# Kernel optimization log

Hardware: AMD Instinct MI355X
Metric: run time of the kernel (lower is better)

## Reference

```python
import jax, jax.numpy as jnp
import numpy as np

DIM = 1024
NUM_HEADS = 16
HEAD_DIM = DIM // NUM_HEADS


def setup_inputs() -> dict:
    key = jax.random.key(0)
    ks = jax.random.split(key, 6)
    B, N, C = 2, 2048, DIM
    s = 1.0 / np.sqrt(C)
    return {
        "x": jax.random.normal(ks[0], (B, N, C), dtype=jnp.float32),
        "Wq": jax.random.normal(ks[1], (C, C), dtype=jnp.float32) * s,
        "Wk": jax.random.normal(ks[2], (C, C), dtype=jnp.float32) * s,
        "Wv": jax.random.normal(ks[3], (C, C), dtype=jnp.float32) * s,
        "Wproj": jax.random.normal(ks[4], (C, C), dtype=jnp.float32) * s,
        "bproj": jax.random.normal(ks[5], (C,), dtype=jnp.float32) * 0.01,
    }


def reference(x, Wq, Wk, Wv, Wproj, bproj):
    B, N, C = x.shape
    H, D = NUM_HEADS, HEAD_DIM
    scale = D ** -0.5
    # Linear (torch convention: y = x @ W.T), then split heads -> [B, H, N, D]
    q = (x @ Wq.T).reshape(B, N, H, D).transpose(0, 2, 1, 3)
    k = (x @ Wk.T).reshape(B, N, H, D).transpose(0, 2, 1, 3)
    v = (x @ Wv.T).reshape(B, N, H, D).transpose(0, 2, 1, 3)
    attn = jnp.einsum("bhnd,bhmd->bhnm", q, k) * scale  # [B,H,N,N]
    attn = jax.nn.softmax(attn, axis=-1)
    out = jnp.einsum("bhnm,bhmd->bhnd", attn, v)  # [B,H,N,D]
    out = out.transpose(0, 2, 1, 3).reshape(B, N, C)
    return out @ Wproj.T + bproj
```

## Files before the change

kernel.cpp:

```cpp
#include <hip/hip_runtime.h>
#include <stdint.h>

typedef unsigned short u16;
typedef unsigned int u32;

typedef __bf16 bf16x8 __attribute__((ext_vector_type(8)));
typedef float f32x4 __attribute__((ext_vector_type(4)));

#define LOG2E_SCALE 0.18033688011112042f

static __device__ __forceinline__ u16 f2bf(float f) {
  union { float f; u32 u; } v; v.f = f;
  u32 r = v.u + 0x7fffu + ((v.u >> 16) & 1u);
  return (u16)(r >> 16);
}
static __device__ __forceinline__ u32 pk2(float a, float b) {
  u32 r;
  asm("v_cvt_pk_bf16_f32 %0, %1, %2" : "=v"(r) : "v"(a), "v"(b));
  return r;
}
static __device__ __forceinline__ float fexp2(float x) {
  return __builtin_amdgcn_exp2f(x);
}
static __device__ __forceinline__ float blo(u32 u) {
  union { u32 u; float f; } v; v.u = u << 16; return v.f;
}
static __device__ __forceinline__ float bhi(u32 u) {
  union { u32 u; float f; } v; v.u = u & 0xffff0000u; return v.f;
}

static __device__ __forceinline__ void gl_lds16(const void* g, void* l) {
  __builtin_amdgcn_global_load_lds(
      (const __attribute__((address_space(1))) u32*)g,
      (__attribute__((address_space(3))) u32*)l, 16, 0, 0);
}

__global__ void cast_kernel(const float* __restrict__ x, const float* __restrict__ wq,
                            const float* __restrict__ wk, const float* __restrict__ wv,
                            const float* __restrict__ wp,
                            u16* __restrict__ xb, u16* __restrict__ wqb, u16* __restrict__ wkb,
                            u16* __restrict__ wvb, u16* __restrict__ wpb) {
  const float* src; u16* dst; int n;
  switch (blockIdx.y) {
    case 0: src = x;  dst = xb;  n = 4194304; break;
    case 1: src = wq; dst = wqb; n = 1048576; break;
    case 2: src = wk; dst = wkb; n = 1048576; break;
    case 3: src = wv; dst = wvb; n = 1048576; break;
    default: src = wp; dst = wpb; n = 1048576; break;
  }
  int i = (blockIdx.x * 256 + threadIdx.x) * 8;
  if (i >= n) return;
  float4 a = *(const float4*)(src + i);
  float4 b = *(const float4*)(src + i + 4);
  uint4 o;
  o.x = pk2(a.x, a.y); o.y = pk2(a.z, a.w);
  o.z = pk2(b.x, b.y); o.w = pk2(b.z, b.w);
  *(uint4*)(dst + i) = o;
}

__global__ __launch_bounds__(256, 3) void gemm_qkv(
    const u16* __restrict__ A, const u16* __restrict__ Bq, const u16* __restrict__ Bk,
    const u16* __restrict__ Bv, u16* __restrict__ oQ, u16* __restrict__ oK,
    u16* __restrict__ oVt)
{
  constexpr int K = 1024;
  __shared__ u16 As[128 * 32];
  __shared__ u16 Bs[128 * 32];
  __shared__ float tbuf[4][16 * 68];

  const int tid  = threadIdx.x;
  const int lane = tid & 63;
  const int wave = tid >> 6;
  const int cl   = lane & 15;
  const int g    = lane >> 4;
  const int wm   = (wave >> 1) * 64;
  const int wn   = (wave & 1) * 64;
  const int bm   = blockIdx.y * 128;
  const int bn   = blockIdx.x * 128;
  const int z    = blockIdx.z;
  const u16* B = (z == 0 ? Bq : (z == 1 ? Bk : Bv));

  f32x4 zero4 = {0.f, 0.f, 0.f, 0.f};
  f32x4 acc[4][4];
#pragma unroll
  for (int i = 0; i < 4; i++)
#pragma unroll
    for (int j = 0; j < 4; j++) acc[i][j] = zero4;

  const int srow = tid >> 2;
  const int sch  = (tid & 3) ^ ((srow >> 1) & 3);
  const char* aG = (const char*)(A + (size_t)(bm + srow) * K) + sch * 16;
  const char* bG = (const char*)(B + (size_t)(bn + srow) * K) + sch * 16;
  char* aL = (char*)As + tid * 16;
  char* bL = (char*)Bs + tid * 16;
  const size_t rstep = (size_t)64 * K * 2;

  const int swz = (cl >> 1) & 3;

  for (int k0 = 0; k0 < K; k0 += 32) {
    gl_lds16(aG + k0 * 2, aL);
    gl_lds16(aG + rstep + k0 * 2, aL + 4096);
    gl_lds16(bG + k0 * 2, bL);
    gl_lds16(bG + rstep + k0 * 2, bL + 4096);
    __syncthreads();

    bf16x8 af[4], bf[4];
#pragma unroll
    for (int i = 0; i < 4; i++)
      af[i] = *(const bf16x8*)(As + (wm + i * 16 + cl) * 32 + ((g ^ swz) & 3) * 8);
#pragma unroll
    for (int j = 0; j < 4; j++)
      bf[j] = *(const bf16x8*)(Bs + (wn + j * 16 + cl) * 32 + ((g ^ swz) & 3) * 8);
#pragma unroll
    for (int i = 0; i < 4; i++)
#pragma unroll
      for (int j = 0; j < 4; j++)
        acc[i][j] = __builtin_amdgcn_mfma_f32_16x16x32_bf16(af[i], bf[j], acc[i][j], 0, 0, 0);
    __syncthreads();
  }

  const int rq = g * 4;
  if (z <= 1) {
    u16* o = z ? oK : oQ;
#pragma unroll
    for (int i = 0; i < 4; i++)
#pragma unroll
      for (int j = 0; j < 4; j++)
#pragma unroll
        for (int r = 0; r < 4; r++) {
          int gm = bm + wm + i * 16 + rq + r;
          int gn = bn + wn + j * 16 + cl;
          int b = gm >> 11, ns = gm & 2047;
          int h = gn >> 6,  d  = gn & 63;
          o[(((size_t)(b * 16 + h)) * 2048 + ns) * 64 + d] = f2bf(acc[i][j][r]);
        }
  } else {
    float* tb = tbuf[wave];
#pragma unroll
    for (int j = 0; j < 4; j++) {
      asm volatile("s_waitcnt lgkmcnt(0)" ::: "memory");
#pragma unroll
      for (int i = 0; i < 4; i++)
        *(f32x4*)(tb + cl * 68 + i * 16 + rq) = acc[i][j];
      asm volatile("s_waitcnt lgkmcnt(0)" ::: "memory");
#pragma unroll
      for (int half = 0; half < 2; half++) {
        int dd = lane >> 2, p = (lane & 3) + half * 4;
        f32x4 x0 = *(const f32x4*)(tb + dd * 68 + p * 8);
        f32x4 x1 = *(const f32x4*)(tb + dd * 68 + p * 8 + 4);
        uint4 pkd;
        pkd.x = pk2(x0[0], x0[1]); pkd.y = pk2(x0[2], x0[3]);
        pkd.z = pk2(x1[0], x1[1]); pkd.w = pk2(x1[2], x1[3]);
        int gn = bn + wn + j * 16 + dd;
        int gm = bm + wm + p * 8;
        int b = gm >> 11, nn = gm & 2047;
        int h = gn >> 6,  dl = gn & 63;
        *(uint4*)(oVt + (((size_t)(b * 16 + h)) * 64 + dl) * 2048 + nn) = pkd;
      }
    }
  }
}

__global__ __launch_bounds__(256, 4) void attn_kernel(
    const u16* __restrict__ Q, const u16* __restrict__ Km,
    const u16* __restrict__ Vt, u16* __restrict__ Op, float* __restrict__ lp)
{
  __shared__ u16 ks[2][64 * 64];
  __shared__ u16 vs[2][64 * 64];
  __shared__ u16 ps[128 * 32];

  const int tid  = threadIdx.x;
  const int lane = tid & 63;
  const int wave = tid >> 6;
  const int cl   = lane & 15;
  const int g    = lane >> 4;
  const int bh   = blockIdx.x;
  const int qt   = blockIdx.y;
  const int sp   = blockIdx.z;

  const char* kS = (const char*)Km + (size_t)bh * 2048 * 128 + (size_t)sp * 1024 * 128;
  const char* vS = (const char*)Vt + (size_t)bh * 64 * 4096 + (size_t)sp * 1024 * 2;

  const u16* qbase = Q + ((size_t)bh * 2048 + qt * 128 + wave * 32) * 64;
  bf16x8 qf[2][2];
#pragma unroll
  for (int i = 0; i < 2; i++)
#pragma unroll
    for (int h = 0; h < 2; h++)
      qf[i][h] = *(const bf16x8*)(qbase + (i * 16 + cl) * 64 + h * 32 + g * 8);

  auto stage_k = [&](int t) {
    const char* kT = kS + (size_t)t * 8192;
    char* dst = (char*)ks[t & 1];
#pragma unroll
    for (int r = 0; r < 2; r++) {
      int c = r * 256 + tid;
      int kv = c >> 3, s = c & 7;
      gl_lds16(kT + kv * 128 + (((s ^ kv) & 7) * 16), dst + c * 16);
    }
  };
  auto stage_v = [&](int t) {
    const char* vT = vS + (size_t)t * 128;
    char* dst = (char*)vs[t & 1];
#pragma unroll
    for (int r = 0; r < 2; r++) {
      int c = r * 256 + tid;
      int d = c >> 3, s = c & 7;
      gl_lds16(vT + (size_t)d * 4096 + (((s ^ d) & 7) * 16), dst + c * 16);
    }
  };

  stage_k(0);
  stage_v(0);

  f32x4 zero4 = {0.f, 0.f, 0.f, 0.f};
  f32x4 o_acc[2][4];
#pragma unroll
  for (int i = 0; i < 2; i++)
#pragma unroll
    for (int j = 0; j < 4; j++) o_acc[i][j] = zero4;
  float li[2] = {0.f, 0.f};

  for (int t = 0; t < 16; ++t) {
    __syncthreads();
    if (t < 15) { stage_k(t + 1); stage_v(t + 1); }

    const u16* kb = ks[t & 1];
    const u16* vb = vs[t & 1];

    f32x4 st[4][2];
#pragma unroll
    for (int j = 0; j < 4; j++) { st[j][0] = zero4; st[j][1] = zero4; }
#pragma unroll
    for (int h = 0; h < 2; h++) {
#pragma unroll
      for (int j = 0; j < 4; j++) {
        bf16x8 kf = *(const bf16x8*)(kb + (j * 16 + cl) * 64 + (((h * 4 + g) ^ (cl & 7)) & 7) * 8);
        st[j][0] = __builtin_amdgcn_mfma_f32_16x16x32_bf16(kf, qf[0][h], st[j][0], 0, 0, 0);
        st[j][1] = __builtin_amdgcn_mfma_f32_16x16x32_bf16(kf, qf[1][h], st[j][1], 0, 0, 0);
      }
    }

#pragma unroll
    for (int i = 0; i < 2; i++) {
      float rs = 0.f;
#pragma unroll
      for (int j = 0; j < 4; j++)
#pragma unroll
        for (int r = 0; r < 4; r++) {
          float p = fexp2(st[j][i][r] * LOG2E_SCALE);
          st[j][i][r] = p;
          rs += p;
        }
      rs += __shfl_xor(rs, 16, 64);
      rs += __shfl_xor(rs, 32, 64);
      li[i] += rs;
    }

#pragma unroll
    for (int h32 = 0; h32 < 2; h32++) {
#pragma unroll
      for (int i = 0; i < 2; i++) {
        int q = wave * 32 + i * 16 + cl;
#pragma unroll
        for (int jj = 0; jj < 2; jj++) {
          int j = h32 * 2 + jj;
          int ch = jj * 2 + (g >> 1);
          int slot = (ch ^ (cl & 3)) & 3;
          uint2 w;
          w.x = pk2(st[j][i][0], st[j][i][1]);
          w.y = pk2(st[j][i][2], st[j][i][3]);
          *(uint2*)((char*)ps + q * 64 + slot * 16 + (g & 1) * 8) = w;
        }
      }
      bf16x8 pf[2], vf[4];
#pragma unroll
      for (int i = 0; i < 2; i++)
        pf[i] = *(const bf16x8*)((const char*)ps + (wave * 32 + i * 16 + cl) * 64 +
                                 ((g ^ (cl & 3)) & 3) * 16);
#pragma unroll
      for (int j = 0; j < 4; j++)
        vf[j] = *(const bf16x8*)(vb + (j * 16 + cl) * 64 + (((h32 * 4 + g) ^ (cl & 7)) & 7) * 8);
#pragma unroll
      for (int i = 0; i < 2; i++)
#pragma unroll
        for (int j = 0; j < 4; j++)
          o_acc[i][j] = __builtin_amdgcn_mfma_f32_16x16x32_bf16(pf[i], vf[j], o_acc[i][j], 0, 0, 0);
    }
  }

  const int b = bh >> 4, hh = bh & 15;
  u16* Os = Op + (size_t)sp * 4194304;
  float* ls = lp + sp * 65536;
#pragma unroll
  for (int i = 0; i < 2; i++) {
    if (g == 0) ls[bh * 2048 + qt * 128 + wave * 32 + i * 16 + cl] = li[i];
#pragma unroll
    for (int r = 0; r < 4; r++) {
      int row = qt * 128 + wave * 32 + i * 16 + g * 4 + r;
      u16* orow = Os + ((size_t)b * 2048 + row) * 1024 + hh * 64;
#pragma unroll
      for (int j = 0; j < 4; j++)
        orow[j * 16 + cl] = f2bf(o_acc[i][j][r]);
    }
  }
}

__global__ void reduce_o(const u16* __restrict__ Op, const float* __restrict__ lp,
                         u16* __restrict__ Ow) {
  int t = blockIdx.x * 256 + threadIdx.x;
  int idx = t * 8;
  int b   = idx >> 21;
  int rem = idx & 2097151;
  int row = rem >> 10;
  int h   = (rem & 1023) >> 6;
  int lidx = (b * 16 + h) * 2048 + row;
  float inv = 1.0f / (lp[lidx] + lp[65536 + lidx]);
  uint4 a = *(const uint4*)(Op + idx);
  uint4 c = *(const uint4*)(Op + 4194304 + idx);
  uint4 o;
  o.x = pk2((blo(a.x) + blo(c.x)) * inv, (bhi(a.x) + bhi(c.x)) * inv);
  o.y = pk2((blo(a.y) + blo(c.y)) * inv, (bhi(a.y) + bhi(c.y)) * inv);
  o.z = pk2((blo(a.z) + blo(c.z)) * inv, (bhi(a.z) + bhi(c.z)) * inv);
  o.w = pk2((blo(a.w) + blo(c.w)) * inv, (bhi(a.w) + bhi(c.w)) * inv);
  *(uint4*)(Ow + idx) = o;
}

__global__ __launch_bounds__(256, 4) void proj_gemm(
    const u16* __restrict__ A, const u16* __restrict__ B,
    float* __restrict__ out, const float* __restrict__ bias)
{
  constexpr int K = 1024;
  __shared__ u16 As[64 * 32];
  __shared__ u16 Bs[128 * 32];

  const int tid  = threadIdx.x;
  const int lane = tid & 63;
  const int wave = tid >> 6;
  const int cl   = lane & 15;
  const int g    = lane >> 4;
  const int wm   = (wave >> 1) * 32;
  const int wn   = (wave & 1) * 64;
  const int bm   = blockIdx.y * 64;
  const int bn   = blockIdx.x * 128;

  f32x4 zero4 = {0.f, 0.f, 0.f, 0.f};
  f32x4 acc[2][4];
#pragma unroll
  for (int i = 0; i < 2; i++)
#pragma unroll
    for (int j = 0; j < 4; j++) acc[i][j] = zero4;

  const int srow = tid >> 2;
  const int sch  = (tid & 3) ^ ((srow >> 1) & 3);
  const char* aG = (const char*)(A + (size_t)(bm + srow) * K) + sch * 16;
  const char* bG = (const char*)(B + (size_t)(bn + srow) * K) + sch * 16;
  char* aL = (char*)As + tid * 16;
  char* bL = (char*)Bs + tid * 16;
  const size_t rstep = (size_t)64 * K * 2;

  const int swz = (cl >> 1) & 3;

  for (int k0 = 0; k0 < K; k0 += 32) {
    gl_lds16(aG + k0 * 2, aL);
    gl_lds16(bG + k0 * 2, bL);
    gl_lds16(bG + rstep + k0 * 2, bL + 4096);
    __syncthreads();

    bf16x8 af[2], bf[4];
#pragma unroll
    for (int i = 0; i < 2; i++)
      af[i] = *(const bf16x8*)(As + (wm + i * 16 + cl) * 32 + ((g ^ swz) & 3) * 8);
#pragma unroll
    for (int j = 0; j < 4; j++)
      bf[j] = *(const bf16x8*)(Bs + (wn + j * 16 + cl) * 32 + ((g ^ swz) & 3) * 8);
#pragma unroll
    for (int i = 0; i < 2; i++)
#pragma unroll
      for (int j = 0; j < 4; j++)
        acc[i][j] = __builtin_amdgcn_mfma_f32_16x16x32_bf16(af[i], bf[j], acc[i][j], 0, 0, 0);
    __syncthreads();
  }

  const int rq = g * 4;
#pragma unroll
  for (int i = 0; i < 2; i++)
#pragma unroll
    for (int j = 0; j < 4; j++)
#pragma unroll
      for (int r = 0; r < 4; r++) {
        int gm = bm + wm + i * 16 + rq + r;
        int gn = bn + wn + j * 16 + cl;
        out[(size_t)gm * 1024 + gn] = acc[i][j][r] + bias[gn];
      }
}

extern "C" void kernel_launch(void* const* d_in, const int* in_sizes, int n_in,
                              void* d_out, int out_size, void* d_ws, size_t ws_size,
                              hipStream_t stream) {
  const float* x     = (const float*)d_in[0];
  const float* Wq    = (const float*)d_in[1];
  const float* Wk    = (const float*)d_in[2];
  const float* Wv    = (const float*)d_in[3];
  const float* Wp    = (const float*)d_in[4];
  const float* bproj = (const float*)d_in[5];

  u16* ws  = (u16*)d_ws;
  u16* xb  = ws;
  u16* wqb = xb + 4194304;
  u16* wkb = wqb + 1048576;
  u16* wvb = wkb + 1048576;
  u16* wpb = wvb + 1048576;
  u16* Qw  = wpb + 1048576;
  u16* Kw  = Qw + 4194304;
  u16* Vw  = Kw + 4194304;
  u16* Ow  = Vw + 4194304;
  u16* Opart = Ow + 4194304;
  float* lpart = (float*)(Opart + 8388608);
  (void)in_sizes; (void)n_in; (void)out_size; (void)ws_size;

  cast_kernel<<<dim3(2048, 5), 256, 0, stream>>>(x, Wq, Wk, Wv, Wp, xb, wqb, wkb, wvb, wpb);
  gemm_qkv<<<dim3(8, 32, 3), 256, 0, stream>>>(xb, wqb, wkb, wvb, Qw, Kw, Vw);
  attn_kernel<<<dim3(32, 16, 2), 256, 0, stream>>>(Qw, Kw, Vw, Opart, lpart);
  reduce_o<<<dim3(2048), 256, 0, stream>>>(Opart, lpart, Ow);
  proj_gemm<<<dim3(8, 64), 256, 0, stream>>>(Ow, wpb, (float*)d_out, bproj);
}
```

Measured before the change: 187.3 us.

## Split attention KV into four chunks with smaller tiles and prescaled Q

Raises the KV split from two to four, so each attention block covers 512 keys in 32-key tiles. LDS shrinks and the launch bound rises to 6 blocks per SU, giving more blocks and higher occupancy. The softmax scale and log2e factor move into the Q projection epilogue, dropping a multiply per score. The cost is a reduce kernel that reads four bf16 partial outputs instead of two, which doubles partial-output traffic, plus more loop iterations with less work per barrier.

```diff
diff --git a/kernel.cpp b/kernel.cpp
--- a/kernel.cpp
+++ b/kernel.cpp
@@ -122,6 +122,7 @@
   const int rq = g * 4;
   if (z <= 1) {
     u16* o = z ? oK : oQ;
+    const float cs = z ? 1.0f : LOG2E_SCALE;
 #pragma unroll
     for (int i = 0; i < 4; i++)
 #pragma unroll
@@ -132,7 +133,7 @@
           int gn = bn + wn + j * 16 + cl;
           int b = gm >> 11, ns = gm & 2047;
           int h = gn >> 6,  d  = gn & 63;
-          o[(((size_t)(b * 16 + h)) * 2048 + ns) * 64 + d] = f2bf(acc[i][j][r]);
+          o[(((size_t)(b * 16 + h)) * 2048 + ns) * 64 + d] = f2bf(acc[i][j][r] * cs);
         }
   } else {
     float* tb = tbuf[wave];
@@ -161,13 +162,13 @@
   }
 }
 
-__global__ __launch_bounds__(256, 4) void attn_kernel(
+__global__ __launch_bounds__(256, 6) void attn_kernel(
     const u16* __restrict__ Q, const u16* __restrict__ Km,
     const u16* __restrict__ Vt, u16* __restrict__ Op, float* __restrict__ lp)
 {
-  __shared__ u16 ks[2][64 * 64];
-  __shared__ u16 vs[2][64 * 64];
-  __shared__ u16 ps[128 * 32];
+  __shared__ u16 ks[2][32 * 64];
+  __shared__ u16 vs[2][64 * 32];
+  __shared__ u16 ps[128 * 36];
 
   const int tid  = threadIdx.x;
   const int lane = tid & 63;
@@ -178,8 +179,8 @@
   const int qt   = blockIdx.y;
   const int sp   = blockIdx.z;
 
-  const char* kS = (const char*)Km + (size_t)bh * 2048 * 128 + (size_t)sp * 1024 * 128;
-  const char* vS = (const char*)Vt + (size_t)bh * 64 * 4096 + (size_t)sp * 1024 * 2;
+  const char* kS = (const char*)Km + (size_t)bh * 2048 * 128 + (size_t)sp * 512 * 128;
+  const char* vS = (const char*)Vt + (size_t)bh * 64 * 4096 + (size_t)sp * 1024;
 
   const u16* qbase = Q + ((size_t)bh * 2048 + qt * 128 + wave * 32) * 64;
   bf16x8 qf[2][2];
@@ -190,24 +191,14 @@
       qf[i][h] = *(const bf16x8*)(qbase + (i * 16 + cl) * 64 + h * 32 + g * 8);
 
   auto stage_k = [&](int t) {
-    const char* kT = kS + (size_t)t * 8192;
-    char* dst = (char*)ks[t & 1];
-#pragma unroll
-    for (int r = 0; r < 2; r++) {
-      int c = r * 256 + tid;
-      int kv = c >> 3, s = c & 7;
-      gl_lds16(kT + kv * 128 + (((s ^ kv) & 7) * 16), dst + c * 16);
-    }
+    const char* kT = kS + (size_t)t * 4096;
+    int kv = tid >> 3, s = tid & 7;
+    gl_lds16(kT + kv * 128 + (((s ^ kv) & 7) * 16), (char*)ks[t & 1] + tid * 16);
   };
   auto stage_v = [&](int t) {
-    const char* vT = vS + (size_t)t * 128;
-    char* dst = (char*)vs[t & 1];
-#pragma unroll
-    for (int r = 0; r < 2; r++) {
-      int c = r * 256 + tid;
-      int d = c >> 3, s = c & 7;
-      gl_lds16(vT + (size_t)d * 4096 + (((s ^ d) & 7) * 16), dst + c * 16);
-    }
+    const char* vT = vS + (size_t)t * 64;
+    int d = tid >> 2, s = tid & 3;
+    gl_lds16(vT + (size_t)d * 4096 + (((s ^ d) & 3) * 16), (char*)vs[t & 1] + tid * 16);
   };
 
   stage_k(0);
@@ -228,13 +219,13 @@
     const u16* kb = ks[t & 1];
     const u16* vb = vs[t & 1];
 
-    f32x4 st[4][2];
-#pragma unroll
-    for (int j = 0; j < 4; j++) { st[j][0] = zero4; st[j][1] = zero4; }
+    f32x4 st[2][2];
+#pragma unroll
+    for (int j = 0; j < 2; j++) { st[j][0] = zero4; st[j][1] = zero4; }
 #pragma unroll
     for (int h = 0; h < 2; h++) {
 #pragma unroll
-      for (int j = 0; j < 4; j++) {
+      for (int j = 0; j < 2; j++) {
         bf16x8 kf = *(const bf16x8*)(kb + (j * 16 + cl) * 64 + (((h * 4 + g) ^ (cl & 7)) & 7) * 8);
         st[j][0] = __builtin_amdgcn_mfma_f32_16x16x32_bf16(kf, qf[0][h], st[j][0], 0, 0, 0);
         st[j][1] = __builtin_amdgcn_mfma_f32_16x16x32_bf16(kf, qf[1][h], st[j][1], 0, 0, 0);
@@ -245,10 +236,10 @@
     for (int i = 0; i < 2; i++) {
       float rs = 0.f;
 #pragma unroll
-      for (int j = 0; j < 4; j++)
+      for (int j = 0; j < 2; j++)
 #pragma unroll
         for (int r = 0; r < 4; r++) {
-          float p = fexp2(st[j][i][r] * LOG2E_SCALE);
+          float p = fexp2(st[j][i][r]);
           st[j][i][r] = p;
           rs += p;
         }
@@ -258,35 +249,34 @@
     }
 
 #pragma unroll
-    for (int h32 = 0; h32 < 2; h32++) {
-#pragma unroll
-      for (int i = 0; i < 2; i++) {
-        int q = wave * 32 + i * 16 + cl;
-#pragma unroll
-        for (int jj = 0; jj < 2; jj++) {
-          int j = h32 * 2 + jj;
-          int ch = jj * 2 + (g >> 1);
-          int slot = (ch ^ (cl & 3)) & 3;
-          uint2 w;
-          w.x = pk2(st[j][i][0], st[j][i][1]);
-          w.y = pk2(st[j][i][2], st[j][i][3]);
-          *(uint2*)((char*)ps + q * 64 + slot * 16 + (g & 1) * 8) = w;
-        }
+    for (int i = 0; i < 2; i++) {
+      char* prow = (char*)ps + (wave * 32 + i * 16 + cl) * 72;
+#pragma unroll
+      for (int j = 0; j < 2; j++) {
+        uint2 w;
+        w.x = pk2(st[j][i][0], st[j][i][1]);
+        w.y = pk2(st[j][i][2], st[j][i][3]);
+        *(uint2*)(prow + j * 32 + g * 8) = w;
       }
-      bf16x8 pf[2], vf[4];
-#pragma unroll
-      for (int i = 0; i < 2; i++)
-        pf[i] = *(const bf16x8*)((const char*)ps + (wave * 32 + i * 16 + cl) * 64 +
-                                 ((g ^ (cl & 3)) & 3) * 16);
+    }
+
+    bf16x8 pf[2], vf[4];
+#pragma unroll
+    for (int i = 0; i < 2; i++) {
+      const char* prow = (const char*)ps + (wave * 32 + i * 16 + cl) * 72;
+      union { bf16x8 v; uint2 u[2]; } pu;
+      pu.u[0] = *(const uint2*)(prow + g * 16);
+      pu.u[1] = *(const uint2*)(prow + g * 16 + 8);
+      pf[i] = pu.v;
+    }
+#pragma unroll
+    for (int j = 0; j < 4; j++)
+      vf[j] = *(const bf16x8*)(vb + (j * 16 + cl) * 32 + (((g ^ (cl & 3)) & 3) * 8));
+#pragma unroll
+    for (int i = 0; i < 2; i++)
 #pragma unroll
       for (int j = 0; j < 4; j++)
-        vf[j] = *(const bf16x8*)(vb + (j * 16 + cl) * 64 + (((h32 * 4 + g) ^ (cl & 7)) & 7) * 8);
-#pragma unroll
-      for (int i = 0; i < 2; i++)
-#pragma unroll
-        for (int j = 0; j < 4; j++)
-          o_acc[i][j] = __builtin_amdgcn_mfma_f32_16x16x32_bf16(pf[i], vf[j], o_acc[i][j], 0, 0, 0);
-    }
+        o_acc[i][j] = __builtin_amdgcn_mfma_f32_16x16x32_bf16(pf[i], vf[j], o_acc[i][j], 0, 0, 0);
   }
 
   const int b = bh >> 4, hh = bh & 15;
@@ -315,14 +305,20 @@
   int row = rem >> 10;
   int h   = (rem & 1023) >> 6;
   int lidx = (b * 16 + h) * 2048 + row;
-  float inv = 1.0f / (lp[lidx] + lp[65536 + lidx]);
-  uint4 a = *(const uint4*)(Op + idx);
-  uint4 c = *(const uint4*)(Op + 4194304 + idx);
+  float inv = 1.0f / (lp[lidx] + lp[65536 + lidx] + lp[131072 + lidx] + lp[196608 + lidx]);
+  uint4 a0 = *(const uint4*)(Op + idx);
+  uint4 a1 = *(const uint4*)(Op + 4194304 + idx);
+  uint4 a2 = *(const uint4*)(Op + 8388608 + idx);
+  uint4 a3 = *(const uint4*)(Op + 12582912 + idx);
   uint4 o;
-  o.x = pk2((blo(a.x) + blo(c.x)) * inv, (bhi(a.x) + bhi(c.x)) * inv);
-  o.y = pk2((blo(a.y) + blo(c.y)) * inv, (bhi(a.y) + bhi(c.y)) * inv);
-  o.z = pk2((blo(a.z) + blo(c.z)) * inv, (bhi(a.z) + bhi(c.z)) * inv);
-  o.w = pk2((blo(a.w) + blo(c.w)) * inv, (bhi(a.w) + bhi(c.w)) * inv);
+  o.x = pk2((blo(a0.x) + blo(a1.x) + blo(a2.x) + blo(a3.x)) * inv,
+            (bhi(a0.x) + bhi(a1.x) + bhi(a2.x) + bhi(a3.x)) * inv);
+  o.y = pk2((blo(a0.y) + blo(a1.y) + blo(a2.y) + blo(a3.y)) * inv,
+            (bhi(a0.y) + bhi(a1.y) + bhi(a2.y) + bhi(a3.y)) * inv);
+  o.z = pk2((blo(a0.z) + blo(a1.z) + blo(a2.z) + blo(a3.z)) * inv,
+            (bhi(a0.z) + bhi(a1.z) + bhi(a2.z) + bhi(a3.z)) * inv);
+  o.w = pk2((blo(a0.w) + blo(a1.w) + blo(a2.w) + blo(a3.w)) * inv,
+            (bhi(a0.w) + bhi(a1.w) + bhi(a2.w) + bhi(a3.w)) * inv);
   *(uint4*)(Ow + idx) = o;
 }
 
@@ -416,12 +412,12 @@
   u16* Vw  = Kw + 4194304;
   u16* Ow  = Vw + 4194304;
   u16* Opart = Ow + 4194304;
-  float* lpart = (float*)(Opart + 8388608);
+  float* lpart = (float*)(Opart + 16777216);
   (void)in_sizes; (void)n_in; (void)out_size; (void)ws_size;
 
   cast_kernel<<<dim3(2048, 5), 256, 0, stream>>>(x, Wq, Wk, Wv, Wp, xb, wqb, wkb, wvb, wpb);
   gemm_qkv<<<dim3(8, 32, 3), 256, 0, stream>>>(xb, wqb, wkb, wvb, Qw, Kw, Vw);
-  attn_kernel<<<dim3(32, 16, 2), 256, 0, stream>>>(Qw, Kw, Vw, Opart, lpart);
+  attn_kernel<<<dim3(32, 16, 4), 256, 0, stream>>>(Qw, Kw, Vw, Opart, lpart);
   reduce_o<<<dim3(2048), 256, 0, stream>>>(Opart, lpart, Ow);
   proj_gemm<<<dim3(8, 64), 256, 0, stream>>>(Ow, wpb, (float*)d_out, bproj);
 }
```

Result: slower. 217.6 us (+16.2%).
